# Kernel optimization log

Measured on AMD Instinct MI355X. Metric: run time of the kernel, lower is better.

## Reference

```python
import jax, jax.numpy as jnp
import numpy as np

N_HEAD = 16
N_EMBD = 1024
BLOCK = 2048
B, T = 4, 2048


def setup_inputs() -> dict:
    key = jax.random.key(0)
    ks = jax.random.split(key, 5)
    s = 0.02
    return {
        "x": jax.random.normal(ks[0], (B, T, N_EMBD), dtype=jnp.float32),
        "qkv_w": jax.random.normal(ks[1], (3 * N_EMBD, N_EMBD), dtype=jnp.float32) * s,
        "qkv_b": jnp.zeros((3 * N_EMBD,), dtype=jnp.float32),
        "proj_w": jax.random.normal(ks[2], (N_EMBD, N_EMBD), dtype=jnp.float32) * s,
        "proj_b": jnp.zeros((N_EMBD,), dtype=jnp.float32),
    }


def reference(x, qkv_w, qkv_b, proj_w, proj_b):
    Bx, Tx, C = x.shape
    hd = C // N_HEAD
    qkv = x @ qkv_w.T + qkv_b  # [B,T,3C]
    q, k, v = jnp.split(qkv, 3, axis=-1)
    # [B,T,C] -> [B,H,T,hd]
    def heads(t):
        return t.reshape(Bx, Tx, N_HEAD, hd).transpose(0, 2, 1, 3)
    q, k, v = heads(q), heads(k), heads(v)
    scores = jnp.einsum("bhqd,bhkd->bhqk", q, k) / jnp.sqrt(jnp.float32(hd))
    causal = jnp.tril(jnp.ones((Tx, Tx), dtype=bool))
    scores = jnp.where(causal[None, None, :, :], scores, -jnp.inf)
    attn = jax.nn.softmax(scores, axis=-1)
    out = jnp.einsum("bhqk,bhkd->bhqd", attn, v)
    out = out.transpose(0, 2, 1, 3).reshape(Bx, Tx, C)
    return out @ proj_w.T + proj_b
```

## Files before the change

kernel.cpp:

```cpp
#include <hip/hip_runtime.h>
#include <stdint.h>
#include <math.h>

#define DEVI __device__ __forceinline__

typedef __attribute__((ext_vector_type(8))) short bf16x8;
typedef __attribute__((ext_vector_type(4))) float f32x4;

DEVI unsigned short f2bf(float f) {
  union { float f; unsigned u; } v; v.f = f;
  unsigned u = v.u;
  u += 0x7fffu + ((u >> 16) & 1u);
  return (unsigned short)(u >> 16);
}

DEVI unsigned cvt_pk_bf16(float a, float b) {
  unsigned r;
  asm("v_cvt_pk_bf16_f32 %0, %1, %2" : "=v"(r) : "v"(a), "v"(b));
  return r;
}

DEVI f32x4 mfma16(bf16x8 a, bf16x8 b, f32x4 c) {
  return __builtin_amdgcn_mfma_f32_16x16x32_bf16(a, b, c, 0, 0, 0);
}

DEVI void gld16(const unsigned short* g, unsigned short* l) {
  __builtin_amdgcn_global_load_lds(
      (const __attribute__((address_space(1))) unsigned int*)(uintptr_t)g,
      (__attribute__((address_space(3))) unsigned int*)(unsigned int)(uintptr_t)l,
      16, 0, 0);
}

#define VMCNT(n) asm volatile("s_waitcnt vmcnt(" #n ")" ::: "memory")
#define BAR()                              \
  do {                                     \
    __builtin_amdgcn_s_barrier();          \
    __builtin_amdgcn_sched_barrier(0);     \
  } while (0)

template <int N> DEVI void vmcntc() {
  static_assert(N >= 0 && N <= 12, "");
  if constexpr (N == 0) VMCNT(0);
  else if constexpr (N == 3) VMCNT(3);
  else if constexpr (N == 4) VMCNT(4);
  else if constexpr (N == 6) VMCNT(6);
  else if constexpr (N == 8) VMCNT(8);
}

__global__ __launch_bounds__(256) void cvt3_kernel(
    const float* __restrict__ a, unsigned short* __restrict__ oa,
    const float* __restrict__ b, unsigned short* __restrict__ ob,
    const float* __restrict__ c, unsigned short* __restrict__ oc) {
  int bid = blockIdx.x;
  const float* in; unsigned short* out; int i;
  if (bid < 8192)       { in = a; out = oa; i = bid; }
  else if (bid < 11264) { in = b; out = ob; i = bid - 8192; }
  else                  { in = c; out = oc; i = bid - 11264; }
  int idx = (i * 256 + (int)threadIdx.x) * 4;
  float4 v = *(const float4*)(in + idx);
  unsigned lo = f2bf(v.x) | ((unsigned)f2bf(v.y) << 16);
  unsigned hi = f2bf(v.z) | ((unsigned)f2bf(v.w) << 16);
  uint2 o; o.x = lo; o.y = hi;
  *(uint2*)(out + idx) = o;
}

template <int MODE, int NBH>
__global__ __launch_bounds__(512, 2) void gemm8(
    const unsigned short* __restrict__ A, const unsigned short* __restrict__ Bw,
    const float* __restrict__ bias, float* __restrict__ Cf,
    unsigned short* __restrict__ Qo, unsigned short* __restrict__ Ko,
    unsigned short* __restrict__ Vo, int M, int N, int K, int nbx) {
  extern __shared__ unsigned short lds[];
  constexpr int BUFS = 8192 + 4096 * NBH;
  constexpr int LPT = 2 + NBH;
  const int tid = threadIdx.x;
  const int lane = tid & 63;
  const int w = tid >> 6;
  const int wm = w >> 2, wn = w & 3;
  const int lr = lane & 15, lq = lane >> 4;

  const int cpx = gridDim.x >> 3;
  const int swz = (blockIdx.x & 7) * cpx + (blockIdx.x >> 3);
  const int bx = swz % nbx, by = swz / nbx;
  const int m0 = by * 256, n0 = bx * (NBH * 128);

  const int srow = lane >> 2;
  const int scol = (((lane & 3) ^ ((lane >> 3) & 3)) << 3);
  const unsigned short* pa = A + (size_t)(m0 + srow) * K + scol;
  const unsigned short* pb = Bw + (size_t)(n0 + srow) * K + scol;

  const int rswz = (lq ^ ((lr >> 1) & 3)) << 3;

  f32x4 acc[8][2 * NBH] = {};

  auto sA = [&](int buf, int kt, int c) {
    gld16(pa + (size_t)(c << 4) * K + kt, lds + buf * BUFS + (c << 9));
  };
  auto sB = [&](int buf, int kt, int c) {
    gld16(pb + (size_t)(c << 4) * K + kt, lds + buf * BUFS + 8192 + (c << 9));
  };
  auto stage = [&](int buf, int t) {
    const int kt = t << 5;
    sA(buf, kt, w); sA(buf, kt, 8 + w);
    sB(buf, kt, w);
    if constexpr (NBH == 2) sB(buf, kt, 8 + w);
  };

  const int NT = K >> 5;
  stage(0, 0); stage(1, 1); stage(2, 2);
  vmcntc<2 * LPT>();
  BAR();

  for (int t = 0; t < NT; ++t) {
    if (t + 3 < NT) stage((t + 3) & 3, t + 3);
    const unsigned short* As_ = lds + (t & 3) * BUFS;
    const unsigned short* Bs_ = As_ + 8192;
    bf16x8 af[8], bf[2 * NBH];
#pragma unroll
    for (int mt = 0; mt < 8; ++mt)
      af[mt] = *(const bf16x8*)(As_ + (wm * 128 + mt * 16 + lr) * 32 + rswz);
#pragma unroll
    for (int nt = 0; nt < 2 * NBH; ++nt)
      bf[nt] = *(const bf16x8*)(Bs_ + (wn * (NBH * 32) + nt * 16 + lr) * 32 + rswz);
    __builtin_amdgcn_s_setprio(1);
#pragma unroll
    for (int mt = 0; mt < 8; ++mt)
#pragma unroll
      for (int nt = 0; nt < 2 * NBH; ++nt)
        acc[mt][nt] = mfma16(af[mt], bf[nt], acc[mt][nt]);
    __builtin_amdgcn_s_setprio(0);
    if (t + 1 < NT) {
      if (t + 3 < NT)      vmcntc<2 * LPT>();
      else if (t + 2 < NT) vmcntc<LPT>();
      else                 vmcntc<0>();
      BAR();
    }
  }

#pragma unroll
  for (int mt = 0; mt < 8; ++mt) {
#pragma unroll
    for (int nt = 0; nt < 2 * NBH; ++nt) {
      int n_g = n0 + wn * (NBH * 32) + nt * 16 + lr;
      float bv = bias[n_g];
      if (MODE == 1) {
#pragma unroll
        for (int r = 0; r < 4; ++r) {
          int m_g = m0 + wm * 128 + mt * 16 + lq * 4 + r;
          Cf[(size_t)m_g * N + n_g] = acc[mt][nt][r] + bv;
        }
      } else {
        int which = n_g >> 10;
        int rem = n_g & 1023;
        int h = rem >> 6, d = rem & 63;
        int m_base = m0 + wm * 128 + mt * 16 + lq * 4;
        int b = m_base >> 11, tt = m_base & 2047;
        if (which == 2) {
          uint2 pv;
          pv.x = cvt_pk_bf16(acc[mt][nt][0] + bv, acc[mt][nt][1] + bv);
          pv.y = cvt_pk_bf16(acc[mt][nt][2] + bv, acc[mt][nt][3] + bv);
          *(uint2*)(Vo + (((size_t)(b * 16 + h) * 64 + d) * 2048 + tt)) = pv;
        } else {
          unsigned short* p = (which == 0) ? Qo : Ko;
#pragma unroll
          for (int r = 0; r < 4; ++r) {
            size_t idx = (((size_t)(b * 16 + h) * 2048) + tt + r) * 64 + d;
            p[idx] = f2bf(acc[mt][nt][r] + bv);
          }
        }
      }
    }
  }
}

__global__ __launch_bounds__(512, 2) void attn_kernel(
    const unsigned short* __restrict__ Q, const unsigned short* __restrict__ K,
    const unsigned short* __restrict__ V, unsigned short* __restrict__ Y) {
  constexpr int T = 2048, HD = 64, H = 16;
  __shared__ unsigned short Kt[2][64 * 72];
  __shared__ unsigned short Vt[2][64 * 72];
  __shared__ unsigned short Pt[8][16 * 72];

  const int tid = threadIdx.x;
  const int lane = tid & 63;
  const int w = tid >> 6;
  const int lr = lane & 15, lq = lane >> 4;
  const int pair = blockIdx.x;
  const int h = blockIdx.y;
  const int b = blockIdx.z;
  const size_t bh = (size_t)(b * H + h) * T * HD;
  const float SC = 0.125f * 1.44269504089f;

  const int krow = tid >> 3, kcb = (tid & 7) << 3;

  float4 kr, vr;
  auto load_tile = [&](int jt) {
    const int c0 = jt * 64;
    kr = *(const float4*)(K + bh + (size_t)(c0 + krow) * HD + kcb);
    vr = *(const float4*)(V + bh + (size_t)krow * T + c0 + kcb);
  };
  auto stage = [&](int buf) {
    *(float4*)(&Kt[buf][krow * 72 + kcb]) = kr;
    *(float4*)(&Vt[buf][krow * 72 + kcb]) = vr;
  };

  load_tile(0);

  for (int phase = 0; phase < 2; ++phase) {
    const int qt = phase ? (7 - pair) : pair;
    const int q0 = qt * 256;
    const int nkv = 4 * (qt + 1);
    const int qw = q0 + w * 32;

    bf16x8 qf[2][2];
#pragma unroll
    for (int qs = 0; qs < 2; ++qs)
#pragma unroll
      for (int kb = 0; kb < 2; ++kb)
        qf[qs][kb] = *(const bf16x8*)(Q + bh + (size_t)(qw + qs * 16 + lr) * HD +
                                      kb * 32 + lq * 8);

    f32x4 o[2][4] = {};
    float mi[2] = {-INFINITY, -INFINITY}, li[2] = {0.f, 0.f};

    stage(0);
    load_tile(1);
    __syncthreads();

    for (int jt = 0; jt < nkv; ++jt) {
      const int c0 = jt * 64;
      const int buf = jt & 1;

      if (c0 <= qw + 31) {
        f32x4 s[2][4];
        __builtin_amdgcn_s_setprio(1);
#pragma unroll
        for (int nt = 0; nt < 4; ++nt) {
          bf16x8 kf0 = *(const bf16x8*)(&Kt[buf][(nt * 16 + lr) * 72 + lq * 8]);
          bf16x8 kf1 = *(const bf16x8*)(&Kt[buf][(nt * 16 + lr) * 72 + 32 + lq * 8]);
#pragma unroll
          for (int qs = 0; qs < 2; ++qs) {
            f32x4 z = {};
            z = mfma16(kf0, qf[qs][0], z);
            s[qs][nt] = mfma16(kf1, qf[qs][1], z);
          }
        }
        __builtin_amdgcn_s_setprio(0);
        if (c0 + 63 > qw) {
#pragma unroll
          for (int qs = 0; qs < 2; ++qs) {
            int qg = qw + qs * 16 + lr;
#pragma unroll
            for (int nt = 0; nt < 4; ++nt)
#pragma unroll
              for (int r = 0; r < 4; ++r) {
                int kvg = c0 + nt * 16 + lq * 4 + r;
                if (kvg > qg) s[qs][nt][r] = -INFINITY;
              }
          }
        }
        float mxs[2];
#pragma unroll
        for (int qs = 0; qs < 2; ++qs) {
          float mx = -INFINITY;
#pragma unroll
          for (int nt = 0; nt < 4; ++nt)
            mx = fmaxf(mx, fmaxf(fmaxf(s[qs][nt][0], s[qs][nt][1]),
                                 fmaxf(s[qs][nt][2], s[qs][nt][3])));
          mx = fmaxf(mx, __shfl_xor(mx, 16));
          mx = fmaxf(mx, __shfl_xor(mx, 32));
          mxs[qs] = mx * SC;
        }
        if (!__all((mxs[0] <= mi[0] + 8.f) && (mxs[1] <= mi[1] + 8.f))) {
#pragma unroll
          for (int qs = 0; qs < 2; ++qs) {
            float mnew = fmaxf(mi[qs], mxs[qs]);
            float alpha = __builtin_amdgcn_exp2f(mi[qs] - mnew);
            mi[qs] = mnew;
            li[qs] *= alpha;
#pragma unroll
            for (int nt = 0; nt < 4; ++nt)
#pragma unroll
              for (int r = 0; r < 4; ++r) o[qs][nt][r] *= alpha;
          }
        }
        bf16x8 pf[2][2];
#pragma unroll
        for (int qs = 0; qs < 2; ++qs) {
          float rs = 0.f;
#pragma unroll
          for (int nt = 0; nt < 4; ++nt) {
            float p0 = __builtin_amdgcn_exp2f(fmaf(s[qs][nt][0], SC, -mi[qs]));
            float p1 = __builtin_amdgcn_exp2f(fmaf(s[qs][nt][1], SC, -mi[qs]));
            float p2 = __builtin_amdgcn_exp2f(fmaf(s[qs][nt][2], SC, -mi[qs]));
            float p3 = __builtin_amdgcn_exp2f(fmaf(s[qs][nt][3], SC, -mi[qs]));
            rs += (p0 + p1) + (p2 + p3);
            uint2 pk;
            pk.x = cvt_pk_bf16(p0, p1);
            pk.y = cvt_pk_bf16(p2, p3);
            *(uint2*)(&Pt[w][lr * 72 + nt * 16 + lq * 4]) = pk;
          }
          li[qs] += rs;
#pragma unroll
          for (int kb = 0; kb < 2; ++kb)
            pf[qs][kb] = *(const bf16x8*)(&Pt[w][lr * 72 + kb * 32 + lq * 8]);
        }
        __builtin_amdgcn_s_setprio(1);
#pragma unroll
        for (int nt = 0; nt < 4; ++nt) {
          bf16x8 vf0 = *(const bf16x8*)(&Vt[buf][(nt * 16 + lr) * 72 + lq * 8]);
          bf16x8 vf1 = *(const bf16x8*)(&Vt[buf][(nt * 16 + lr) * 72 + 32 + lq * 8]);
#pragma unroll
          for (int qs = 0; qs < 2; ++qs) {
            o[qs][nt] = mfma16(vf0, pf[qs][0], o[qs][nt]);
            o[qs][nt] = mfma16(vf1, pf[qs][1], o[qs][nt]);
          }
        }
        __builtin_amdgcn_s_setprio(0);
      }

      if (jt + 1 < nkv) {
        stage(buf ^ 1);
        if (jt + 2 < nkv) load_tile(jt + 2);
        else if (phase == 0) load_tile(0);
        __syncthreads();
      }
    }

#pragma unroll
    for (int qs = 0; qs < 2; ++qs) {
      float l = li[qs];
      l += __shfl_xor(l, 16);
      l += __shfl_xor(l, 32);
      float inv = 1.f / l;
      int t_g = qw + qs * 16 + lr;
#pragma unroll
      for (int nt = 0; nt < 4; ++nt) {
        uint2 yv;
        yv.x = cvt_pk_bf16(o[qs][nt][0] * inv, o[qs][nt][1] * inv);
        yv.y = cvt_pk_bf16(o[qs][nt][2] * inv, o[qs][nt][3] * inv);
        *(uint2*)(Y + ((size_t)(b * T + t_g)) * 1024 + h * 64 + nt * 16 + lq * 4) = yv;
      }
    }
  }
}

extern "C" void kernel_launch(void* const* d_in, const int* in_sizes, int n_in,
                              void* d_out, int out_size, void* d_ws, size_t ws_size,
                              hipStream_t stream) {
  const float* x = (const float*)d_in[0];
  const float* qkv_w = (const float*)d_in[1];
  const float* qkv_b = (const float*)d_in[2];
  const float* proj_w = (const float*)d_in[3];
  const float* proj_b = (const float*)d_in[4];
  float* out = (float*)d_out;

  unsigned short* ws = (unsigned short*)d_ws;
  unsigned short* xb = ws;
  unsigned short* wqkv = xb + 8388608;
  unsigned short* wproj = wqkv + 3145728;
  unsigned short* Qb = wproj + 1048576;
  unsigned short* Kb = Qb + 8388608;
  unsigned short* Vb = Kb + 8388608;
  unsigned short* Yb = Vb + 8388608;

  auto* g0 = gemm8<0, 2>;
  auto* g1 = gemm8<1, 1>;
  static bool attr_set = false;
  if (!attr_set) {
    (void)hipFuncSetAttribute((const void*)g0,
                              hipFuncAttributeMaxDynamicSharedMemorySize, 131072);
    (void)hipFuncSetAttribute((const void*)g1,
                              hipFuncAttributeMaxDynamicSharedMemorySize, 98304);
    attr_set = true;
  }

  cvt3_kernel<<<12288, 256, 0, stream>>>(x, xb, qkv_w, wqkv, proj_w, wproj);

  gemm8<0, 2><<<dim3(384), 512, 131072, stream>>>(xb, wqkv, qkv_b, nullptr, Qb, Kb,
                                                  Vb, 8192, 3072, 1024, 12);
  attn_kernel<<<dim3(4, 16, 4), 512, 0, stream>>>(Qb, Kb, Vb, Yb);
  gemm8<1, 1><<<dim3(256), 512, 98304, stream>>>(Yb, wproj, proj_b, out, nullptr,
                                                 nullptr, nullptr, 8192, 1024, 1024, 8);
}
```

Measured before the change: 252.5 us.

## Restructure GEMM main loop into double-buffered K=64 quadrant-interleaved pipeline

Replaces the 4-stage K=32 ring buffer in the bf16 GEMM with two K=64 buffers and a new XOR swizzle. Each tile is staged in quarter-tile pieces (A/B halves) interleaved with the matching quadrant MFMA blocks, with barriers between phases in a ping-pong schedule. The goal is to overlap global-to-LDS loads and LDS reads with MFMA work at a finer grain and to halve the loop iteration overhead. In exchange there are many more barriers per tile, larger LDS use per buffer, and the launch must supply the matching shared-memory size.

```diff
diff --git a/kernel.cpp b/kernel.cpp
--- a/kernel.cpp
+++ b/kernel.cpp
@@ -34,17 +34,16 @@
 #define VMCNT(n) asm volatile("s_waitcnt vmcnt(" #n ")" ::: "memory")
 #define BAR()                              \
   do {                                     \
+    __builtin_amdgcn_sched_barrier(0);     \
     __builtin_amdgcn_s_barrier();          \
     __builtin_amdgcn_sched_barrier(0);     \
   } while (0)
 
 template <int N> DEVI void vmcntc() {
-  static_assert(N >= 0 && N <= 12, "");
+  static_assert(N >= 0 && N <= 8, "");
   if constexpr (N == 0) VMCNT(0);
   else if constexpr (N == 3) VMCNT(3);
   else if constexpr (N == 4) VMCNT(4);
-  else if constexpr (N == 6) VMCNT(6);
-  else if constexpr (N == 8) VMCNT(8);
 }
 
 __global__ __launch_bounds__(256) void cvt3_kernel(
@@ -71,8 +70,8 @@
     unsigned short* __restrict__ Qo, unsigned short* __restrict__ Ko,
     unsigned short* __restrict__ Vo, int M, int N, int K, int nbx) {
   extern __shared__ unsigned short lds[];
-  constexpr int BUFS = 8192 + 4096 * NBH;
-  constexpr int LPT = 2 + NBH;
+  constexpr int BUFS = 16384 + 8192 * NBH;
+  constexpr int GATE = 2 + NBH;
   const int tid = threadIdx.x;
   const int lane = tid & 63;
   const int w = tid >> 6;
@@ -84,58 +83,123 @@
   const int bx = swz % nbx, by = swz / nbx;
   const int m0 = by * 256, n0 = bx * (NBH * 128);
 
-  const int srow = lane >> 2;
-  const int scol = (((lane & 3) ^ ((lane >> 3) & 3)) << 3);
-  const unsigned short* pa = A + (size_t)(m0 + srow) * K + scol;
-  const unsigned short* pb = Bw + (size_t)(n0 + srow) * K + scol;
-
-  const int rswz = (lq ^ ((lr >> 1) & 3)) << 3;
+  const int sr = lane >> 3;
+  const int sc = ((lane & 7) ^ sr) << 3;
+  const unsigned short* pa = A + (size_t)(m0 + sr) * K + sc;
+  const unsigned short* pb = Bw + (size_t)(n0 + sr) * K + sc;
+
+  const int bs0 = (lq ^ (lr & 7)) << 3;
+  const int bs1 = ((lq + 4) ^ (lr & 7)) << 3;
 
   f32x4 acc[8][2 * NBH] = {};
 
   auto sA = [&](int buf, int kt, int c) {
-    gld16(pa + (size_t)(c << 4) * K + kt, lds + buf * BUFS + (c << 9));
+    gld16(pa + (size_t)(c << 3) * K + kt, lds + buf * BUFS + (c << 9));
   };
   auto sB = [&](int buf, int kt, int c) {
-    gld16(pb + (size_t)(c << 4) * K + kt, lds + buf * BUFS + 8192 + (c << 9));
-  };
-  auto stage = [&](int buf, int t) {
-    const int kt = t << 5;
-    sA(buf, kt, w); sA(buf, kt, 8 + w);
-    sB(buf, kt, w);
-    if constexpr (NBH == 2) sB(buf, kt, 8 + w);
-  };
-
-  const int NT = K >> 5;
-  stage(0, 0); stage(1, 1); stage(2, 2);
-  vmcntc<2 * LPT>();
+    gld16(pb + (size_t)(c << 3) * K + kt, lds + buf * BUFS + 16384 + (c << 9));
+  };
+  auto sAa = [&](int buf, int kt) { sA(buf, kt, w); sA(buf, kt, 16 + w); };
+  auto sAb = [&](int buf, int kt) { sA(buf, kt, 8 + w); sA(buf, kt, 24 + w); };
+  auto sBa = [&](int buf, int kt) {
+    if constexpr (NBH == 2) {
+      int c = (w & 3) + ((w >> 2) << 3);
+      sB(buf, kt, c); sB(buf, kt, c + 16);
+    } else {
+      sB(buf, kt, ((w & 3) << 2) + (w >> 2));
+    }
+  };
+  auto sBb = [&](int buf, int kt) {
+    if constexpr (NBH == 2) {
+      int c = (w & 3) + ((w >> 2) << 3) + 4;
+      sB(buf, kt, c); sB(buf, kt, c + 16);
+    } else {
+      sB(buf, kt, ((w & 3) << 2) + (w >> 2) + 2);
+    }
+  };
+
+#define LDA(A_, As_, mh)                                                     \
+  _Pragma("unroll") for (int i = 0; i < 4; ++i) {                            \
+    int ar = wm * 128 + (mh) * 64 + i * 16 + lr;                             \
+    A_[i][0] = *(const bf16x8*)((As_) + ar * 64 + bs0);                      \
+    A_[i][1] = *(const bf16x8*)((As_) + ar * 64 + bs1);                      \
+  }
+#define LDB(B_, Bs_, nh)                                                     \
+  _Pragma("unroll") for (int j = 0; j < NBH; ++j) {                          \
+    int br = wn * (NBH * 32) + (nh) * (NBH * 16) + j * 16 + lr;              \
+    B_[j][0] = *(const bf16x8*)((Bs_) + br * 64 + bs0);                      \
+    B_[j][1] = *(const bf16x8*)((Bs_) + br * 64 + bs1);                      \
+  }
+#define MM(A_, B_, mh, nh)                                                   \
+  __builtin_amdgcn_s_setprio(1);                                             \
+  _Pragma("unroll") for (int i = 0; i < 4; ++i)                              \
+    _Pragma("unroll") for (int j = 0; j < NBH; ++j) {                        \
+      acc[(mh) * 4 + i][(nh) * NBH + j] = mfma16(                            \
+          A_[i][0], B_[j][0], acc[(mh) * 4 + i][(nh) * NBH + j]);            \
+      acc[(mh) * 4 + i][(nh) * NBH + j] = mfma16(                            \
+          A_[i][1], B_[j][1], acc[(mh) * 4 + i][(nh) * NBH + j]);            \
+    }                                                                        \
+  __builtin_amdgcn_s_setprio(0);
+
+  const int NT = K >> 6;
+  const int NI = NT >> 1;
+  const unsigned short* As0 = lds;
+  const unsigned short* Bs0 = lds + 16384;
+  const unsigned short* As1 = lds + BUFS;
+  const unsigned short* Bs1 = lds + BUFS + 16384;
+
+  sAa(0, 0); sBb(0, 0); sBa(0, 0); sAb(0, 0);
+  sAa(1, 64); sBb(1, 64);
+  vmcntc<GATE>();
   BAR();
 
-  for (int t = 0; t < NT; ++t) {
-    if (t + 3 < NT) stage((t + 3) & 3, t + 3);
-    const unsigned short* As_ = lds + (t & 3) * BUFS;
-    const unsigned short* Bs_ = As_ + 8192;
-    bf16x8 af[8], bf[2 * NBH];
-#pragma unroll
-    for (int mt = 0; mt < 8; ++mt)
-      af[mt] = *(const bf16x8*)(As_ + (wm * 128 + mt * 16 + lr) * 32 + rswz);
-#pragma unroll
-    for (int nt = 0; nt < 2 * NBH; ++nt)
-      bf[nt] = *(const bf16x8*)(Bs_ + (wn * (NBH * 32) + nt * 16 + lr) * 32 + rswz);
-    __builtin_amdgcn_s_setprio(1);
-#pragma unroll
-    for (int mt = 0; mt < 8; ++mt)
-#pragma unroll
-      for (int nt = 0; nt < 2 * NBH; ++nt)
-        acc[mt][nt] = mfma16(af[mt], bf[nt], acc[mt][nt]);
-    __builtin_amdgcn_s_setprio(0);
-    if (t + 1 < NT) {
-      if (t + 3 < NT)      vmcntc<2 * LPT>();
-      else if (t + 2 < NT) vmcntc<LPT>();
-      else                 vmcntc<0>();
-      BAR();
-    }
-  }
+  for (int i = 0; i < NI; ++i) {
+    const bool more = (i + 1 < NI);
+    const int kt1 = (2 * i + 1) << 6;
+    const int kt2 = (2 * i + 2) << 6;
+    const int kt3 = (2 * i + 3) << 6;
+    bf16x8 af[4][2], b0f[NBH][2], b1f[NBH][2];
+    sBa(1, kt1);
+    LDA(af, As0, 0); LDB(b0f, Bs0, 0);
+    BAR();
+    MM(af, b0f, 0, 0);
+    BAR();
+    sAb(1, kt1);
+    LDB(b1f, Bs0, 1);
+    BAR();
+    MM(af, b1f, 0, 1);
+    BAR();
+    if (more) sAa(0, kt2);
+    LDA(af, As0, 1);
+    BAR();
+    MM(af, b1f, 1, 1);
+    BAR();
+    if (more) sBb(0, kt2);
+    MM(af, b0f, 1, 0);
+    if (more) { vmcntc<GATE>(); } else { vmcntc<0>(); }
+    BAR();
+    if (more) sBa(0, kt2);
+    LDA(af, As1, 0); LDB(b0f, Bs1, 0);
+    BAR();
+    MM(af, b0f, 0, 0);
+    BAR();
+    if (more) sAb(0, kt2);
+    LDB(b1f, Bs1, 1);
+    BAR();
+    MM(af, b1f, 0, 1);
+    BAR();
+    if (more) sAa(1, kt3);
+    LDA(af, As1, 1);
+    BAR();
+    MM(af, b1f, 1, 1);
+    BAR();
+    if (more) sBb(1, kt3);
+    MM(af, b0f, 1, 0);
+    if (more) { vmcntc<GATE>(); BAR(); }
+  }
+#undef LDA
+#undef LDB
+#undef MM
 
 #pragma unroll
   for (int mt = 0; mt < 8; ++mt) {
```

Measured after the change: 247.4 us. -2.0%, faster.
